# Kernel optimization log

Hardware: AMD Instinct MI355X
Metric: run time of the kernel (lower is better)

Reference implementation:

```python
import jax, jax.numpy as jnp
import numpy as np

NUM_SEGMENTS = 256  # B = batch_keys.max()+1, static for jit


def setup_inputs() -> dict:
    key = jax.random.key(0)
    k1, k2 = jax.random.split(key)
    N, L, D = 2048, 512, 256
    protein_embeds = jax.random.normal(k1, (N, L, D), dtype=jnp.float32)
    # sorted random segment ids in [0, NUM_SEGMENTS); guarantee every segment
    # is non-empty (the torch code skips empty keys, changing output shape;
    # we keep all segments populated so the output is a static [B, D]).
    base = jnp.arange(NUM_SEGMENTS, dtype=jnp.int64)
    rest = jax.random.randint(k2, (N - NUM_SEGMENTS,), 0, NUM_SEGMENTS, dtype=jnp.int64)
    batch_keys = jnp.sort(jnp.concatenate([base, rest]))
    return {"protein_embeds": protein_embeds, "batch_keys": batch_keys}


def reference(protein_embeds, batch_keys):
    # protein_embeds: [N, L, D] float32; batch_keys: [N] int64 in [0, B)
    # Pooling method 'mean': for each key b, nanmean over ALL tokens of all
    # proteins with that key (flattened along the sequence dim). Inputs have
    # no NaNs, so nanmean == mean = segment_sum / segment_count.
    N, L, D = protein_embeds.shape
    tokens = protein_embeds.reshape(N * L, D)            # [N*L, D]
    seg = jnp.repeat(batch_keys, L)                      # token-level segment ids
    sums = jax.ops.segment_sum(tokens, seg, num_segments=NUM_SEGMENTS)  # [B, D]
    counts = jax.ops.segment_sum(jnp.ones((N * L,), tokens.dtype), seg,
                                 num_segments=NUM_SEGMENTS)             # [B]
    return sums / counts[:, None]
```

## Files before the change

### kernel.cpp

```cpp
#include <hip/hip_runtime.h>
#include <hip/hip_bf16.h>

#define N_PROT 2048
#define L_SEQ  512
#define D_DIM  256
#define B_SEG  256
#define SPLIT  2
#define ROWS_PER_BLK (L_SEQ / SPLIT)

__global__ __launch_bounds__(256) void seg_sum_kernel(const float* __restrict__ x,
                                                      const int* __restrict__ keys,
                                                      float* __restrict__ out) {
    const int blk  = blockIdx.x;
    const int prot = blk >> 1;
    const int part = blk & (SPLIT - 1);
    const int tid  = threadIdx.x;
    const int dq   = tid & 63;
    const int r    = tid >> 6;

    const float4* row_base = (const float4*)(x + (size_t)(prot * L_SEQ + part * ROWS_PER_BLK) * D_DIM);
    float4 acc = make_float4(0.f, 0.f, 0.f, 0.f);
    #pragma unroll 4
    for (int l = r; l < ROWS_PER_BLK; l += 4) {
        float4 v = row_base[(size_t)l * (D_DIM / 4) + dq];
        acc.x += v.x; acc.y += v.y; acc.z += v.z; acc.w += v.w;
    }

    __shared__ float4 lds[256];
    lds[tid] = acc;
    __syncthreads();
    if (r == 0) {
        float4 a = lds[dq];
        float4 b = lds[dq + 64];
        float4 c = lds[dq + 128];
        float4 d = lds[dq + 192];
        float sx = (a.x + b.x) + (c.x + d.x);
        float sy = (a.y + b.y) + (c.y + d.y);
        float sz = (a.z + b.z) + (c.z + d.z);
        float sw = (a.w + b.w) + (c.w + d.w);
        const int key = keys[prot];
        float* o = out + (size_t)key * D_DIM + dq * 4;
        atomicAdd(o + 0, sx);
        atomicAdd(o + 1, sy);
        atomicAdd(o + 2, sz);
        atomicAdd(o + 3, sw);
    }
}

__global__ __launch_bounds__(256) void finalize_kernel(const int* __restrict__ keys,
                                                       float* __restrict__ out) {
    const int b = blockIdx.x;
    const int d = threadIdx.x;

    int lo = 0, hi = N_PROT;
    while (lo < hi) { int mid = (lo + hi) >> 1; if (keys[mid] <  b) lo = mid + 1; else hi = mid; }
    const int start = lo;
    lo = start; hi = N_PROT;
    while (lo < hi) { int mid = (lo + hi) >> 1; if (keys[mid] <= b) lo = mid + 1; else hi = mid; }
    const int cnt_tokens = (lo - start) * L_SEQ;

    const float inv = 1.0f / (float)cnt_tokens;
    out[(size_t)b * D_DIM + d] *= inv;
}

extern "C" void kernel_launch(void* const* d_in, const int* in_sizes, int n_in,
                              void* d_out, int out_size, void* d_ws, size_t ws_size,
                              hipStream_t stream) {
    const float* x    = (const float*)d_in[0];
    const int*   keys = (const int*)d_in[1];
    float* out        = (float*)d_out;

    hipMemsetAsync(out, 0, (size_t)out_size * sizeof(float), stream);

    seg_sum_kernel<<<N_PROT * SPLIT, 256, 0, stream>>>(x, keys, out);
    finalize_kernel<<<B_SEG, 256, 0, stream>>>(keys, out);
}
```

Measured before the change: 1.318 ms.

## Replace atomic segment accumulation with per-part workspace partials and gather reduce

The first kernel now writes per-block, per-row-group partial sums into a workspace instead of reducing through LDS and issuing global float atomics. The second kernel finds each segment's protein range and sums that segment's partial rows before dividing by the count. This removes the memset, the LDS barrier and the atomic contention, and the inner loop now uses two accumulators for more loads in flight. In exchange it adds workspace traffic (about 16 MB written and read back) and a serial per-segment loop in the final kernel.

```diff
diff --git a/kernel.cpp b/kernel.cpp
--- a/kernel.cpp
+++ b/kernel.cpp
@@ -1,5 +1,4 @@
 #include <hip/hip_runtime.h>
-#include <hip/hip_bf16.h>
 
 #define N_PROT 2048
 #define L_SEQ  512
@@ -7,47 +6,35 @@
 #define B_SEG  256
 #define SPLIT  2
 #define ROWS_PER_BLK (L_SEQ / SPLIT)
+#define RG 4
+#define PARTS_PER_PROT (SPLIT * RG)
 
-__global__ __launch_bounds__(256) void seg_sum_kernel(const float* __restrict__ x,
-                                                      const int* __restrict__ keys,
-                                                      float* __restrict__ out) {
-    const int blk  = blockIdx.x;
-    const int prot = blk >> 1;
-    const int part = blk & (SPLIT - 1);
-    const int tid  = threadIdx.x;
-    const int dq   = tid & 63;
-    const int r    = tid >> 6;
+__global__ __launch_bounds__(256) void part_sum_kernel(const float* __restrict__ x,
+                                                       float* __restrict__ ws) {
+    const int blk = blockIdx.x;
+    const int tid = threadIdx.x;
+    const int dq  = tid & 63;
+    const int r   = tid >> 6;
 
-    const float4* row_base = (const float4*)(x + (size_t)(prot * L_SEQ + part * ROWS_PER_BLK) * D_DIM);
-    float4 acc = make_float4(0.f, 0.f, 0.f, 0.f);
+    const float4* base = (const float4*)x + (size_t)blk * ROWS_PER_BLK * (D_DIM / 4);
+
+    float4 a0 = make_float4(0.f, 0.f, 0.f, 0.f);
+    float4 a1 = make_float4(0.f, 0.f, 0.f, 0.f);
     #pragma unroll 4
-    for (int l = r; l < ROWS_PER_BLK; l += 4) {
-        float4 v = row_base[(size_t)l * (D_DIM / 4) + dq];
-        acc.x += v.x; acc.y += v.y; acc.z += v.z; acc.w += v.w;
+    for (int l = r; l < ROWS_PER_BLK; l += 2 * RG) {
+        float4 v0 = base[(size_t)l * (D_DIM / 4) + dq];
+        float4 v1 = base[(size_t)(l + RG) * (D_DIM / 4) + dq];
+        a0.x += v0.x; a0.y += v0.y; a0.z += v0.z; a0.w += v0.w;
+        a1.x += v1.x; a1.y += v1.y; a1.z += v1.z; a1.w += v1.w;
     }
+    float4 s = make_float4(a0.x + a1.x, a0.y + a1.y, a0.z + a1.z, a0.w + a1.w);
 
-    __shared__ float4 lds[256];
-    lds[tid] = acc;
-    __syncthreads();
-    if (r == 0) {
-        float4 a = lds[dq];
-        float4 b = lds[dq + 64];
-        float4 c = lds[dq + 128];
-        float4 d = lds[dq + 192];
-        float sx = (a.x + b.x) + (c.x + d.x);
-        float sy = (a.y + b.y) + (c.y + d.y);
-        float sz = (a.z + b.z) + (c.z + d.z);
-        float sw = (a.w + b.w) + (c.w + d.w);
-        const int key = keys[prot];
-        float* o = out + (size_t)key * D_DIM + dq * 4;
-        atomicAdd(o + 0, sx);
-        atomicAdd(o + 1, sy);
-        atomicAdd(o + 2, sz);
-        atomicAdd(o + 3, sw);
-    }
+    float4* wsr = (float4*)ws + (size_t)(blk * RG + r) * (D_DIM / 4);
+    wsr[dq] = s;
 }
 
-__global__ __launch_bounds__(256) void finalize_kernel(const int* __restrict__ keys,
+__global__ __launch_bounds__(256) void seg_mean_kernel(const float* __restrict__ ws,
+                                                       const int* __restrict__ keys,
                                                        float* __restrict__ out) {
     const int b = blockIdx.x;
     const int d = threadIdx.x;
@@ -55,12 +42,19 @@
     int lo = 0, hi = N_PROT;
     while (lo < hi) { int mid = (lo + hi) >> 1; if (keys[mid] <  b) lo = mid + 1; else hi = mid; }
     const int start = lo;
-    lo = start; hi = N_PROT;
+    hi = N_PROT;
     while (lo < hi) { int mid = (lo + hi) >> 1; if (keys[mid] <= b) lo = mid + 1; else hi = mid; }
-    const int cnt_tokens = (lo - start) * L_SEQ;
+    const int end = lo;
 
-    const float inv = 1.0f / (float)cnt_tokens;
-    out[(size_t)b * D_DIM + d] *= inv;
+    const int row0 = start * PARTS_PER_PROT;
+    const int row1 = end   * PARTS_PER_PROT;
+
+    float s = 0.f;
+    for (int rr = row0; rr < row1; ++rr)
+        s += ws[(size_t)rr * D_DIM + d];
+
+    const float cnt_tokens = (float)((end - start) * L_SEQ);
+    out[(size_t)b * D_DIM + d] = s / cnt_tokens;
 }
 
 extern "C" void kernel_launch(void* const* d_in, const int* in_sizes, int n_in,
@@ -69,9 +63,8 @@
     const float* x    = (const float*)d_in[0];
     const int*   keys = (const int*)d_in[1];
     float* out        = (float*)d_out;
+    float* ws         = (float*)d_ws;
 
-    hipMemsetAsync(out, 0, (size_t)out_size * sizeof(float), stream);
-
-    seg_sum_kernel<<<N_PROT * SPLIT, 256, 0, stream>>>(x, keys, out);
-    finalize_kernel<<<B_SEG, 256, 0, stream>>>(keys, out);
+    part_sum_kernel<<<N_PROT * SPLIT, 256, 0, stream>>>(x, ws);
+    seg_mean_kernel<<<B_SEG, 256, 0, stream>>>(ws, keys, out);
 }
```

After: 1.367 ms. +3.7%, slower.
